# Kernel tuning notes

Measured on AMD Instinct MI355X. Metric: run time of the kernel, lower is better.

The kernel has to match this reference:

```python
import jax, jax.numpy as jnp
import numpy as np

CONF_THRES = 0.1
IOU_THRES = 0.6
MAX_DET = 300
MAX_WH = 4096.0  # class offset for non-agnostic NMS
NEG_SLOPE = 0.01  # nn.LeakyReLU default


def xywh2xyxy(p):
    xy, wh = p[..., :2], p[..., 2:4]
    return jnp.concatenate([xy - wh / 2, xy + wh / 2], axis=-1)


def pairwise_iou(a, b):
    area_a = (a[:, 2] - a[:, 0]) * (a[:, 3] - a[:, 1])
    area_b = (b[:, 2] - b[:, 0]) * (b[:, 3] - b[:, 1])
    lt = jnp.maximum(a[:, None, :2], b[None, :, :2])
    rb = jnp.minimum(a[:, None, 2:], b[None, :, 2:])
    wh = jnp.clip(rb - lt, 0.0)
    inter = wh[..., 0] * wh[..., 1]
    return inter / (area_a[:, None] + area_b[None, :] - inter + 1e-7)


def nms_single(pred):  # pred: [N, 5+nc]
    boxes = xywh2xyxy(pred[:, :4])
    scores = pred[:, 5:] * pred[:, 4:5]  # obj * cls
    conf = jnp.max(scores, axis=1)
    cls = jnp.argmax(scores, axis=1)
    conf = jnp.where(conf > CONF_THRES, conf, 0.0)
    topv, topi = jax.lax.top_k(conf, MAX_DET)
    b = boxes[topi]                      # [K,4]
    c = cls[topi]
    valid = topv > CONF_THRES
    bo = b + (c.astype(b.dtype) * MAX_WH)[:, None]  # class-offset boxes
    iou = pairwise_iou(bo, bo)           # [K,K]
    idx = jnp.arange(MAX_DET)
    def body(i, keep):
        sup = keep[i] & (iou[i] > IOU_THRES) & (idx > i)
        return keep & ~sup
    keep = jax.lax.fori_loop(0, MAX_DET, body, valid)
    return b, keep


def bilinear_sample(feat, y, x):  # feat [C,H,W], y/x [K,P] -> [C,K,P]
    C, H, W = feat.shape
    y = jnp.clip(y, 0.0, H - 1.0)
    x = jnp.clip(x, 0.0, W - 1.0)
    y0 = jnp.floor(y).astype(jnp.int32)
    x0 = jnp.floor(x).astype(jnp.int32)
    y1 = jnp.minimum(y0 + 1, H - 1)
    x1 = jnp.minimum(x0 + 1, W - 1)
    ly = y - y0
    lx = x - x0
    return (feat[:, y0, x0] * ((1 - ly) * (1 - lx))
            + feat[:, y0, x1] * ((1 - ly) * lx)
            + feat[:, y1, x0] * (ly * (1 - lx))
            + feat[:, y1, x1] * (ly * lx))


def roi_align_1x1(feat, boxes, scale):  # feat [C,H,W], boxes [K,4] xyxy (input-px)
    b = boxes * scale
    w = jnp.maximum(b[:, 2] - b[:, 0], 1.0)
    h = jnp.maximum(b[:, 3] - b[:, 1], 1.0)
    off = jnp.array([0.5, 1.5], dtype=boxes.dtype)
    xs = b[:, 0:1] + off[None, :] * (w[:, None] / 2.0)  # [K,2]
    ys = b[:, 1:2] + off[None, :] * (h[:, None] / 2.0)
    yy = ys[:, jnp.array([0, 0, 1, 1])]  # [K,4] 2x2 grid
    xx = xs[:, jnp.array([0, 1, 0, 1])]
    v = bilinear_sample(feat, yy, xx)    # [C,K,4]
    return jnp.mean(v, axis=2).T         # [K,C]


def rescale_boxes(bbox, hw, hw0):  # scale_coords + normalize by orig shape
    gain = jnp.minimum(hw[0] / hw0[0], hw[1] / hw0[1])
    pad_x = (hw[1] - hw0[1] * gain) / 2.0
    pad_y = (hw[0] - hw0[0] * gain) / 2.0
    x1 = jnp.clip((bbox[:, 0] - pad_x) / gain, 0.0, hw0[1])
    y1 = jnp.clip((bbox[:, 1] - pad_y) / gain, 0.0, hw0[0])
    x2 = jnp.clip((bbox[:, 2] - pad_x) / gain, 0.0, hw0[1])
    y2 = jnp.clip((bbox[:, 3] - pad_y) / gain, 0.0, hw0[0])
    # divide by shapes[i][0] indexed [w,h,w,h]
    return jnp.stack([x1 / hw0[1], y1 / hw0[0], x2 / hw0[1], y2 / hw0[0]], axis=1)


def setup_inputs() -> dict:
    key = jax.random.key(0)
    ks = jax.random.split(key, 10)
    B, N, NC = 8, 25500, 80
    xy = jax.random.uniform(ks[0], (B, N, 2), minval=0.0, maxval=640.0)
    wh = jax.random.uniform(ks[1], (B, N, 2), minval=8.0, maxval=160.0)
    obj = jax.random.uniform(ks[2], (B, N, 1))
    cls = jax.random.uniform(ks[3], (B, N, NC))
    preds = jnp.concatenate([xy, wh, obj, cls], axis=-1)
    feat1 = jax.random.normal(ks[4], (B, 128, 80, 80), dtype=jnp.float32)
    feat2 = jax.random.normal(ks[5], (B, 256, 40, 40), dtype=jnp.float32)
    feat3 = jax.random.normal(ks[6], (B, 512, 20, 20), dtype=jnp.float32)
    feat4 = jax.random.normal(ks[7], (B, 1024, 10, 10), dtype=jnp.float32)
    orig_hw = jnp.tile(jnp.array([[720.0, 1280.0]], dtype=jnp.float32), (B, 1))
    W1 = jax.random.normal(ks[8], (1920, 256), dtype=jnp.float32) * 0.02
    b1 = jnp.zeros((256,), dtype=jnp.float32)
    W2 = jax.random.normal(ks[9], (256, 256), dtype=jnp.float32) * 0.02
    b2 = jnp.zeros((256,), dtype=jnp.float32)
    return {"preds": preds, "feat1": feat1, "feat2": feat2, "feat3": feat3,
            "feat4": feat4, "orig_hw": orig_hw, "W1": W1, "b1": b1,
            "W2": W2, "b2": b2}


def reference(preds, feat1, feat2, feat3, feat4, orig_hw, W1, b1, W2, b2):
    preds = jax.lax.stop_gradient(preds)  # out.detach() in the original
    hw = jnp.array(feat1.shape[-2:], dtype=preds.dtype) * 8.0  # network input h,w
    boxes, keep = jax.vmap(nms_single)(preds)  # [B,K,4], [B,K]
    f1 = jax.vmap(lambda f, b: roi_align_1x1(f, b, 1.0 / 8))(feat1, boxes)
    f2 = jax.vmap(lambda f, b: roi_align_1x1(f, b, 1.0 / 16))(feat2, boxes)
    f3 = jax.vmap(lambda f, b: roi_align_1x1(f, b, 1.0 / 32))(feat3, boxes)
    f4 = jax.vmap(lambda f, b: roi_align_1x1(f, b, 1.0 / 64))(feat4, boxes)
    f = jnp.concatenate([f1, f2, f3, f4], axis=-1)  # [B,K,1920]
    h = jax.nn.leaky_relu(f @ W1 + b1, NEG_SLOPE)
    h = jax.nn.leaky_relu(h @ W2 + b2, NEG_SLOPE)   # [B,K,256]
    bb = jax.vmap(lambda b, s: rescale_boxes(b, hw, s))(boxes, orig_hw)
    out = jnp.concatenate([bb, h], axis=-1)  # [B,K,260]
    return out * keep[..., None].astype(out.dtype)
```

## Files before the change

### kernel.cpp

```cpp
#include <hip/hip_runtime.h>
#include <hip/hip_bf16.h>
#include <cstdint>
#include <cstddef>

#define NBATCH 8
#define NANCH 25500
#define MAXDET 300
#define NBINS 2048
#define SCAT_BLKS 64

typedef __bf16 bf16x8 __attribute__((ext_vector_type(8)));
typedef float floatx4 __attribute__((ext_vector_type(4)));
typedef unsigned long long ull;

__device__ __forceinline__ int conf_bin(float v) {
  unsigned bits = __float_as_uint(v);
  int bin = (int)((bits - 0x3D800000u) >> 14);
  return bin > (NBINS - 1) ? (NBINS - 1) : bin;
}

#define CONF_TILE 64
__global__ __launch_bounds__(256) void conf_kernel(const float* __restrict__ preds,
                                                   float* __restrict__ conf,
                                                   int* __restrict__ cls,
                                                   int* __restrict__ zmem, int zints,
                                                   int total) {
  if (blockIdx.x < 33) {
    int base = blockIdx.x * 1024;
    #pragma unroll
    for (int k = 0; k < 4; ++k) {
      int i = base + k * 256 + threadIdx.x;
      if (i < zints) zmem[i] = 0;
    }
  }
  __shared__ float s[CONF_TILE * 85];
  int base = blockIdx.x * CONF_TILE;
  int nA = total - base; if (nA > CONF_TILE) nA = CONF_TILE;
  int n4 = (nA * 85) >> 2;
  const float4* g4 = (const float4*)(preds + (size_t)base * 85);
  float4* s4 = (float4*)s;
  for (int i = threadIdx.x; i < n4; i += 256) s4[i] = g4[i];
  __syncthreads();
  int lane16 = threadIdx.x & 15;
  int sub = threadIdx.x >> 4;
  #pragma unroll
  for (int r = 0; r < 4; ++r) {
    int a = r * 16 + sub;
    if (a < nA) {
      const float* row = s + a * 85;
      float obj = row[4];
      float best = -1.0f; int bc = 0;
      #pragma unroll
      for (int j = 0; j < 5; ++j) {
        int c = lane16 * 5 + j;
        float v = row[5 + c] * obj;
        if (v > best) { best = v; bc = c; }
      }
      #pragma unroll
      for (int m = 1; m < 16; m <<= 1) {
        float ov = __shfl_xor(best, m, 64);
        int   oc = __shfl_xor(bc,   m, 64);
        if (ov > best || (ov == best && oc < bc)) { best = ov; bc = oc; }
      }
      if (lane16 == 0) {
        int idx = base + a;
        conf[idx] = (best > 0.1f) ? best : 0.0f;
        cls[idx] = bc;
      }
    }
  }
}

struct TransArgs {
  const float* src[6];
  __hip_bfloat16* dst[6];
  int C[6], HW[6], tx[6], tpb[6], start[6];
};

__global__ __launch_bounds__(256) void trans_scatter_kernel(TransArgs a,
                                                            const float* __restrict__ conf,
                                                            const float* __restrict__ preds,
                                                            const int* __restrict__ clsg,
                                                            int* __restrict__ ghist,
                                                            int* __restrict__ gcnt,
                                                            int* __restrict__ ctr1,
                                                            float* __restrict__ gV,
                                                            int* __restrict__ gI,
                                                            float4* __restrict__ gBox) {
  #pragma clang fp contract(off)
  __shared__ __align__(16) char smem[8448];
  int bid = blockIdx.x;
  int t = threadIdx.y * 32 + threadIdx.x;

  if (bid < SCAT_BLKS) {
    int b = bid >> 3, seg = bid & 7;
    int* s_h = (int*)smem;
    int* shv = (int*)(smem + 8192);
    #pragma unroll
    for (int k = 0; k < 8; ++k) s_h[t + k * 256] = 0;
    if (t == 0) shv[0] = NBINS;
    __syncthreads();
    const int N4 = NANCH >> 2;
    int i0 = (N4 * seg) >> 3, i1 = (N4 * (seg + 1)) >> 3;
    const float4* cf4 = (const float4*)(conf + (size_t)b * NANCH);
    for (int i = i0 + t; i < i1; i += 256) {
      float4 v = cf4[i];
      if (v.x > 0.1f) atomicAdd(&s_h[conf_bin(v.x)], 1);
      if (v.y > 0.1f) atomicAdd(&s_h[conf_bin(v.y)], 1);
      if (v.z > 0.1f) atomicAdd(&s_h[conf_bin(v.z)], 1);
      if (v.w > 0.1f) atomicAdd(&s_h[conf_bin(v.w)], 1);
    }
    __syncthreads();
    #pragma unroll
    for (int k = 0; k < 8; ++k) {
      int bin = t + k * 256;
      int c = s_h[bin];
      if (c) atomicAdd(&ghist[b * NBINS + bin], c);
    }
    __syncthreads();
    if (t == 0) {
      __threadfence();
      atomicAdd(&ctr1[b], 1);
      while (atomicAdd(&ctr1[b], 0) < 8) __builtin_amdgcn_s_sleep(2);
      __threadfence();
    }
    __syncthreads();
    int r[8], suf[8], rs[8];
    int w = t >> 6, lane = t & 63;
    {
      #pragma unroll
      for (int k = 0; k < 8; ++k)
        r[k] = atomicAdd(&ghist[b * NBINS + (w * 8 + k) * 64 + lane], 0);
      int bsum = 0;
      #pragma unroll
      for (int k = 0; k < 8; ++k) {
        int s = r[k];
        #pragma unroll
        for (int d = 1; d < 64; d <<= 1) {
          int o = __shfl_down(s, d, 64);
          if (lane + d < 64) s += o;
        }
        suf[k] = s - r[k];
        rs[k] = __shfl(s, 0, 64);
        bsum += rs[k];
      }
      if (lane == 0) shv[4 + w] = bsum;
    }
    __syncthreads();
    {
      int p1 = shv[5], p2 = shv[6], p3 = shv[7];
      int total = shv[4] + p1 + p2 + p3;
      int target = total < 300 ? total : 300;
      int RS = (w == 0) ? (p1 + p2 + p3) : (w == 1) ? (p2 + p3) : (w == 2) ? p3 : 0;
      int run = RS;
      #pragma unroll
      for (int k = 7; k >= 0; --k) {
        int Sx = run + suf[k] + r[k];
        int Sx1 = Sx - r[k];
        int bin = (w * 8 + k) * 64 + lane;
        s_h[bin] = Sx1;
        if (total > 0 && Sx >= target && Sx1 < target) shv[0] = bin;
        run += rs[k];
      }
    }
    __syncthreads();
    int T = shv[0];
    for (int i = i0 + t; i < i1; i += 256) {
      float4 v4 = cf4[i];
      int ib = i * 4;
      float vv[4] = {v4.x, v4.y, v4.z, v4.w};
      #pragma unroll
      for (int q = 0; q < 4; ++q) {
        float v = vv[q];
        if (v > 0.1f) {
          int bin = conf_bin(v);
          if (bin >= T) {
            int slot = s_h[bin] + atomicAdd(&gcnt[b * NBINS + bin], 1);
            int idx = ib + q;
            const float* p = preds + ((size_t)b * NANCH + idx) * 85;
            float cx = p[0], cy = p[1], wq = p[2], hq = p[3];
            float hw2 = wq * 0.5f, hh2 = hq * 0.5f;
            float x1 = cx - hw2, y1 = cy - hh2, x2 = cx + hw2, y2 = cy + hh2;
            int c = clsg[(size_t)b * NANCH + idx];
            size_t g = (size_t)b * NANCH + slot;
            gV[g] = v;
            gI[g] = idx | (c << 20);
            gBox[g] = make_float4(x1, y1, x2, y2);
          }
        }
      }
    }
    return;
  }

  {
    float (*tile)[33] = (float(*)[33])smem;
    int bid2 = bid - SCAT_BLKS;
    int s = 0;
    #pragma unroll
    for (int i = 1; i < 6; ++i) if (bid2 >= a.start[i]) s = i;
    int local = bid2 - a.start[s];
    int C = a.C[s], HW = a.HW[s], tx0 = a.tx[s], tpb = a.tpb[s];
    int b = local / tpb;
    int rem = local - b * tpb;
    int p0 = (rem % tx0) * 32;
    int c0 = (rem / tx0) * 32;
    const float* inb = a.src[s] + (size_t)b * C * HW;
    __hip_bfloat16* outb = a.dst[s] + (size_t)b * C * HW;
    int tx = threadIdx.x, ty = threadIdx.y;
    #pragma unroll
    for (int k = 0; k < 32; k += 8) {
      int c = c0 + ty + k, p = p0 + tx;
      if (c < C && p < HW) tile[ty + k][tx] = inb[(size_t)c * HW + p];
    }
    __syncthreads();
    #pragma unroll
    for (int k = 0; k < 32; k += 8) {
      int p = p0 + ty + k, c = c0 + tx;
      if (p < HW && c < C) outb[(size_t)p * C + c] = __float2bfloat16(tile[tx][ty + k]);
    }
  }
}

__global__ __launch_bounds__(1024) void nms_kernel(const float* __restrict__ gV,
                                                   const int* __restrict__ gI,
                                                   const float4* __restrict__ gBox,
                                                   const int* __restrict__ ghist,
                                                   float* __restrict__ boxesWs, int* __restrict__ keepWs,
                                                   const float* __restrict__ orig_hw,
                                                   float* __restrict__ out) {
  #pragma clang fp contract(off)
  __shared__ __align__(16) char smem[30208];
  int*    s_h  = (int*)smem;
  float4* bo4  = (float4*)(smem + 8192);
  float (*bxx)[4] = (float(*)[4])(smem + 12992);
  ull   (*mask)[5] = (ull(*)[5])(smem + 17792);
  ull* keepw = (ull*)(smem + 29792);
  ull* nzrow = (ull*)(smem + 29832);
  int* shv   = (int*)(smem + 29872);
  int b = blockIdx.x;
  int t = threadIdx.x;

  if (t < 300) {
    bo4[t] = make_float4(0.0f, 0.0f, 0.0f, 0.0f);
    bxx[t][0] = 0.0f; bxx[t][1] = 0.0f; bxx[t][2] = 0.0f; bxx[t][3] = 0.0f;
  }
  if (t < 5) nzrow[t] = 0ULL;
  if (t == 0) { shv[0] = NBINS; shv[2] = 0; }
  {
    int r[8], suf[8], rs[8];
    int w = t >> 6, lane = t & 63;
    if (t < 256) {
      #pragma unroll
      for (int k = 0; k < 8; ++k)
        r[k] = ghist[b * NBINS + (w * 8 + k) * 64 + lane];
      int bsum = 0;
      #pragma unroll
      for (int k = 0; k < 8; ++k) {
        int s = r[k];
        #pragma unroll
        for (int d = 1; d < 64; d <<= 1) {
          int o = __shfl_down(s, d, 64);
          if (lane + d < 64) s += o;
        }
        suf[k] = s - r[k];
        rs[k] = __shfl(s, 0, 64);
        bsum += rs[k];
      }
      if (lane == 0) shv[4 + w] = bsum;
    }
    __syncthreads();
    if (t < 256) {
      int p1 = shv[5], p2 = shv[6], p3 = shv[7];
      int total = shv[4] + p1 + p2 + p3;
      int target = total < 300 ? total : 300;
      int RS = (w == 0) ? (p1 + p2 + p3) : (w == 1) ? (p2 + p3) : (w == 2) ? p3 : 0;
      int run = RS;
      #pragma unroll
      for (int k = 7; k >= 0; --k) {
        int Sx = run + suf[k] + r[k];
        int Sx1 = Sx - r[k];
        int bin = (w * 8 + k) * 64 + lane;
        s_h[bin] = Sx;
        if (total > 0 && Sx >= target && Sx1 < target) { shv[0] = bin; shv[2] = Sx; }
        run += rs[k];
      }
      if (t == 0) shv[1] = total;
    }
  }
  __syncthreads();
  int total = shv[1];
  int Kslots = shv[2];
  int nvalid = total < 300 ? total : 300;

  if (t >= nvalid && t < 300) {
    size_t bi = ((size_t)(b * 300 + t)) * 4;
    boxesWs[bi + 0] = 0.0f; boxesWs[bi + 1] = 0.0f;
    boxesWs[bi + 2] = 0.0f; boxesWs[bi + 3] = 0.0f;
  }
  if (t < 5) {
    int n = nvalid - t * 64;
    keepw[t] = (n <= 0) ? 0ULL : (n >= 64 ? ~0ULL : ((1ULL << n) - 1ULL));
  }

  {
    const float* vb = gV + (size_t)b * NANCH;
    const int*   ib2 = gI + (size_t)b * NANCH;
    for (int sIdx = t; sIdx < Kslots; sIdx += 1024) {
      float v = vb[sIdx];
      unsigned code = (unsigned)ib2[sIdx];
      int id = (int)(code & 0xFFFFFu);
      int bin = conf_bin(v);
      int lo = (bin + 1 < NBINS) ? s_h[bin + 1] : 0;
      int hi = s_h[bin];
      int rank = lo;
      for (int j = lo; j < hi; ++j) {
        float vj = vb[j];
        int ij = ib2[j] & 0xFFFFF;
        int gt = vj > v;
        int eq = (vj == v) & (ij < id);
        rank += gt | eq;
      }
      if (rank < 300) {
        float4 bx = gBox[(size_t)b * NANCH + sIdx];
        bxx[rank][0] = bx.x; bxx[rank][1] = bx.y; bxx[rank][2] = bx.z; bxx[rank][3] = bx.w;
        size_t bi = ((size_t)(b * 300 + rank)) * 4;
        boxesWs[bi + 0] = bx.x; boxesWs[bi + 1] = bx.y;
        boxesWs[bi + 2] = bx.z; boxesWs[bi + 3] = bx.w;
        int c = (int)(code >> 20);
        float off = (float)c * 4096.0f;
        float4 ob; ob.x = bx.x + off; ob.y = bx.y + off; ob.z = bx.z + off; ob.w = bx.w + off;
        bo4[rank] = ob;
      }
    }
  }
  __syncthreads();

  {
    int wv2 = t >> 6, ln = t & 63;
    if (wv2 < 10) {
      int w2 = wv2 >> 1, half = wv2 & 1;
      int j = w2 * 64 + ln;
      int jc = j < 300 ? j : 0;
      float4 jb = bo4[jc];
      float ja = (jb.z - jb.x) * (jb.w - jb.y);
      bool jv = j < 300;
      int iend = w2 * 64 + 64; if (iend > 300) iend = 300;
      int i0 = half * 150, i1 = i0 + 150; if (i1 > iend) i1 = iend;
      #pragma unroll 4
      for (int i = i0; i < i1; ++i) {
        float4 ib = bo4[i];
        float ai = (ib.z - ib.x) * (ib.w - ib.y);
        float ltx = fmaxf(ib.x, jb.x);
        float lty = fmaxf(ib.y, jb.y);
        float rbx = fminf(ib.z, jb.z);
        float rby = fminf(ib.w, jb.w);
        float wx = fmaxf(rbx - ltx, 0.0f);
        float wy = fmaxf(rby - lty, 0.0f);
        float inter = wx * wy;
        float iou = inter / (ai + ja - inter + 1e-7f);
        ull bal = __ballot(jv && (j > i) && (iou > 0.6f));
        if (ln == 0) {
          mask[i][w2] = bal;
          if (bal) atomicOr(&nzrow[i >> 6], 1ULL << (i & 63));
        }
      }
    }
  }
  __syncthreads();
  if (t == 0) {
    ull kw[5], nz[5];
    #pragma unroll
    for (int w2 = 0; w2 < 5; ++w2) { kw[w2] = keepw[w2]; nz[w2] = nzrow[w2]; }
    #pragma unroll
    for (int w2 = 0; w2 < 5; ++w2) {
      ull p = kw[w2] & nz[w2];
      while (p) {
        int l2 = __builtin_ctzll(p);
        p &= p - 1;
        int i = w2 * 64 + l2;
        for (int w3 = w2; w3 < 5; ++w3) {
          ull m = mask[i][w3];
          kw[w3] &= ~m;
          if (w3 == w2) p &= ~m;
        }
      }
    }
    #pragma unroll
    for (int w2 = 0; w2 < 5; ++w2) keepw[w2] = kw[w2];
  }
  __syncthreads();
  if (t < 300) {
    int kp = (int)((keepw[t >> 6] >> (t & 63)) & 1ULL);
    keepWs[b * 300 + t] = kp;
    float oh = orig_hw[b * 2 + 0], ow = orig_hw[b * 2 + 1];
    float gain = fminf(640.0f / oh, 640.0f / ow);
    float padx = (640.0f - ow * gain) * 0.5f;
    float pady = (640.0f - oh * gain) * 0.5f;
    float x1 = fminf(fmaxf((bxx[t][0] - padx) / gain, 0.0f), ow) / ow;
    float y1 = fminf(fmaxf((bxx[t][1] - pady) / gain, 0.0f), oh) / oh;
    float x2 = fminf(fmaxf((bxx[t][2] - padx) / gain, 0.0f), ow) / ow;
    float y2 = fminf(fmaxf((bxx[t][3] - pady) / gain, 0.0f), oh) / oh;
    size_t o = ((size_t)(b * 300 + t)) * 260;
    out[o + 0] = kp ? x1 : 0.0f;
    out[o + 1] = kp ? y1 : 0.0f;
    out[o + 2] = kp ? x2 : 0.0f;
    out[o + 3] = kp ? y2 : 0.0f;
  }
}

__global__ __launch_bounds__(256) void roi_kernel(const float* __restrict__ boxes,
                                                  const __hip_bfloat16* __restrict__ fT1, const __hip_bfloat16* __restrict__ fT2,
                                                  const __hip_bfloat16* __restrict__ fT3, const __hip_bfloat16* __restrict__ fT4,
                                                  __hip_bfloat16* __restrict__ f) {
  int b = blockIdx.x & 7;
  int r = blockIdx.x >> 3;
  __shared__ int t_off[4][16];
  __shared__ float t_w[4][16];
  int t = threadIdx.x;
  const int Hs[4] = {80, 40, 20, 10};
  const int Cs[4] = {128, 256, 512, 1024};
  const float ss[4] = {0.125f, 0.0625f, 0.03125f, 0.015625f};
  size_t bbase = ((size_t)(b * 300 + r)) * 4;
  float bx0 = boxes[bbase + 0];
  float by0 = boxes[bbase + 1];
  float bx1 = boxes[bbase + 2];
  float by1 = boxes[bbase + 3];
  if (t < 64) {
    int lv = t >> 4, k = t & 15, pp = k >> 2, nb = k & 3;
    float s = ss[lv];
    int H = Hs[lv], W = Hs[lv], C = Cs[lv];
    float b0 = bx0 * s, b1 = by0 * s, b2 = bx1 * s, b3 = by1 * s;
    float w = fmaxf(b2 - b0, 1.0f), h = fmaxf(b3 - b1, 1.0f);
    const float offv[2] = {0.5f, 1.5f};
    float px = b0 + offv[pp & 1] * (w * 0.5f);
    float py = b1 + offv[pp >> 1] * (h * 0.5f);
    float y = fminf(fmaxf(py, 0.0f), (float)(H - 1));
    float x = fminf(fmaxf(px, 0.0f), (float)(W - 1));
    int y0 = (int)floorf(y), x0 = (int)floorf(x);
    int y1 = min(y0 + 1, H - 1), x1 = min(x0 + 1, W - 1);
    float ly = y - (float)y0, lx = x - (float)x0;
    int yy = (nb & 2) ? y1 : y0;
    int xx = (nb & 1) ? x1 : x0;
    float wy = (nb & 2) ? ly : (1.0f - ly);
    float wx = (nb & 1) ? lx : (1.0f - lx);
    t_off[lv][k] = (yy * W + xx) * C;
    t_w[lv][k] = wy * wx;
  }
  __syncthreads();
  const __hip_bfloat16* bases[4] = {
    fT1 + (size_t)b * 6400 * 128,
    fT2 + (size_t)b * 1600 * 256,
    fT3 + (size_t)b * 400 * 512,
    fT4 + (size_t)b * 100 * 1024
  };
  __hip_bfloat16* frow = f + (size_t)(b * 300 + r) * 1920;
  int cbase = 0;
  #pragma unroll
  for (int lv = 0; lv < 4; ++lv) {
    int C = Cs[lv];
    const __hip_bfloat16* base = bases[lv];
    for (int c = t; c < C; c += 256) {
      float acc = 0.0f;
      #pragma unroll
      for (int k = 0; k < 16; ++k)
        acc += t_w[lv][k] * __bfloat162float(base[t_off[lv][k] + c]);
      frow[cbase + c] = __float2bfloat16(acc * 0.25f);
    }
    cbase += C;
  }
}

#define GLDS16(gp, lp) __builtin_amdgcn_global_load_lds( \
    (const __attribute__((address_space(1))) unsigned int*)(gp), \
    (__attribute__((address_space(3))) unsigned int*)(lp), 16, 0, 0)

__global__ __launch_bounds__(256) void gemm_tile_kernel(const __hip_bfloat16* __restrict__ A,
                                                        const __hip_bfloat16* __restrict__ BT,
                                                        const float* __restrict__ bias,
                                                        __hip_bfloat16* __restrict__ Cb,
                                                        float* __restrict__ Cf,
                                                        const int* __restrict__ keep,
                                                        int M, int N, int K, int ldc, int coff) {
  __shared__ __hip_bfloat16 sA[2][64 * 64];
  __shared__ __hip_bfloat16 sB[2][64 * 64];
  int tid = threadIdx.x;
  int bm = blockIdx.x * 64, bn = blockIdx.y * 64;
  int wave = tid >> 6, lane = tid & 63;
  int wr = wave >> 1, wc = wave & 1;
  int idx16 = lane & 15, kb = lane >> 4;
  floatx4 acc[2][2] = {};
  int nt = K >> 6;

  auto stage = [&](int buf, int t) {
    int k0 = t << 6;
    #pragma unroll
    for (int i = 0; i < 2; ++i) {
      int c = tid + i * 256;
      int row = c >> 3, cc = c & 7;
      int scc = cc ^ (row & 7);
      GLDS16(A + (size_t)(bm + row) * K + k0 + scc * 8,
             (char*)&sA[buf][0] + c * 16);
    }
    #pragma unroll
    for (int i = 0; i < 2; ++i) {
      int c = tid + i * 256;
      int row = c >> 3, cc = c & 7;
      int scc = cc ^ (row & 7);
      GLDS16(BT + (size_t)(bn + row) * K + k0 + scc * 8,
             (char*)&sB[buf][0] + c * 16);
    }
  };

  stage(0, 0);
  asm volatile("s_waitcnt vmcnt(0)" ::: "memory");
  __syncthreads();
  int cur = 0;
  for (int t = 0; t < nt; ++t) {
    if (t + 1 < nt) stage(cur ^ 1, t + 1);
    const char* Ab = (const char*)&sA[cur][0];
    const char* Bb = (const char*)&sB[cur][0];
    #pragma unroll
    for (int s = 0; s < 2; ++s) {
      bf16x8 af[2], bg[2];
      #pragma unroll
      for (int m = 0; m < 2; ++m) {
        int row = wr * 32 + m * 16 + idx16;
        int chunk = s * 4 + kb;
        af[m] = *(const bf16x8*)(Ab + row * 128 + ((chunk ^ (row & 7)) * 16));
      }
      #pragma unroll
      for (int n = 0; n < 2; ++n) {
        int row = wc * 32 + n * 16 + idx16;
        int chunk = s * 4 + kb;
        bg[n] = *(const bf16x8*)(Bb + row * 128 + ((chunk ^ (row & 7)) * 16));
      }
      #pragma unroll
      for (int m = 0; m < 2; ++m)
        #pragma unroll
        for (int n = 0; n < 2; ++n)
          acc[m][n] = __builtin_amdgcn_mfma_f32_16x16x32_bf16(af[m], bg[n], acc[m][n], 0, 0, 0);
    }
    asm volatile("s_waitcnt vmcnt(0)" ::: "memory");
    __syncthreads();
    cur ^= 1;
  }
  int col = lane & 15, rb4 = (lane >> 4) * 4;
  #pragma unroll
  for (int m = 0; m < 2; ++m) {
    #pragma unroll
    for (int n = 0; n < 2; ++n) {
      #pragma unroll
      for (int r = 0; r < 4; ++r) {
        int orow = bm + wr * 32 + m * 16 + rb4 + r;
        int ocol = bn + wc * 32 + n * 16 + col;
        if (orow >= M) continue;
        float v = acc[m][n][r] + bias[ocol];
        v = (v >= 0.0f) ? v : 0.01f * v;
        if (Cb) Cb[(size_t)orow * N + ocol] = __float2bfloat16(v);
        if (Cf) {
          float km = keep ? (keep[orow] ? 1.0f : 0.0f) : 1.0f;
          Cf[(size_t)orow * ldc + coff + ocol] = v * km;
        }
      }
    }
  }
}

extern "C" void kernel_launch(void* const* d_in, const int* in_sizes, int n_in,
                              void* d_out, int out_size, void* d_ws, size_t ws_size,
                              hipStream_t stream) {
  (void)in_sizes; (void)n_in; (void)out_size; (void)ws_size;
  const float* preds  = (const float*)d_in[0];
  const float* feat1  = (const float*)d_in[1];
  const float* feat2  = (const float*)d_in[2];
  const float* feat3  = (const float*)d_in[3];
  const float* feat4  = (const float*)d_in[4];
  const float* orighw = (const float*)d_in[5];
  const float* W1     = (const float*)d_in[6];
  const float* b1     = (const float*)d_in[7];
  const float* W2     = (const float*)d_in[8];
  const float* b2     = (const float*)d_in[9];
  float* out = (float*)d_out;

  char* ws = (char*)d_ws;
  size_t off = 0;
  auto alloc = [&](size_t bytes) -> void* {
    void* p = ws + off;
    off = (off + bytes + 255) & ~(size_t)255;
    return p;
  };
  const int BN = NBATCH * NANCH;
  float*  conf   = (float*)alloc((size_t)BN * 4);
  int*    cls    = (int*)  alloc((size_t)BN * 4);
  float*  gV     = (float*)alloc((size_t)BN * 4);
  int*    gI     = (int*)  alloc((size_t)BN * 4);
  float4* gBox   = (float4*)alloc((size_t)BN * 16);
  int*    ghist  = (int*)  alloc((size_t)NBATCH * NBINS * 4);
  int*    gcnt   = (int*)  alloc((size_t)NBATCH * NBINS * 4);
  int*    ctr1   = (int*)  alloc(256);
  const int zints = NBATCH * NBINS * 2 + 64;
  float*  boxes  = (float*)alloc((size_t)NBATCH * 300 * 4 * 4);
  int*    keep   = (int*)  alloc((size_t)NBATCH * 300 * 4);
  __hip_bfloat16* fT1  = (__hip_bfloat16*)alloc((size_t)NBATCH * 6400 * 128 * 2);
  __hip_bfloat16* fT2  = (__hip_bfloat16*)alloc((size_t)NBATCH * 1600 * 256 * 2);
  __hip_bfloat16* fT3  = (__hip_bfloat16*)alloc((size_t)NBATCH * 400 * 512 * 2);
  __hip_bfloat16* fT4  = (__hip_bfloat16*)alloc((size_t)NBATCH * 100 * 1024 * 2);
  __hip_bfloat16* fmat = (__hip_bfloat16*)alloc((size_t)2400 * 1920 * 2);
  __hip_bfloat16* h1b  = (__hip_bfloat16*)alloc((size_t)2400 * 256 * 2);
  __hip_bfloat16* W1T  = (__hip_bfloat16*)alloc((size_t)256 * 1920 * 2);
  __hip_bfloat16* W2T  = (__hip_bfloat16*)alloc((size_t)256 * 256 * 2);

  conf_kernel<<<(BN + CONF_TILE - 1) / CONF_TILE, 256, 0, stream>>>(preds, conf, cls,
                                                                    ghist, zints, BN);

  TransArgs ta;
  ta.src[0] = feat1; ta.dst[0] = fT1; ta.C[0] = 128;  ta.HW[0] = 6400; ta.tx[0] = 200;
  ta.src[1] = feat2; ta.dst[1] = fT2; ta.C[1] = 256;  ta.HW[1] = 1600; ta.tx[1] = 50;
  ta.src[2] = feat3; ta.dst[2] = fT3; ta.C[2] = 512;  ta.HW[2] = 400;  ta.tx[2] = 13;
  ta.src[3] = feat4; ta.dst[3] = fT4; ta.C[3] = 1024; ta.HW[3] = 100;  ta.tx[3] = 4;
  ta.src[4] = W1;    ta.dst[4] = W1T; ta.C[4] = 1920; ta.HW[4] = 256;  ta.tx[4] = 8;
  ta.src[5] = W2;    ta.dst[5] = W2T; ta.C[5] = 256;  ta.HW[5] = 256;  ta.tx[5] = 8;
  int n_tiles = 0;
  for (int s = 0; s < 6; ++s) {
    int ty = (ta.C[s] + 31) / 32;
    int nbatch = (s < 4) ? NBATCH : 1;
    ta.tpb[s] = ta.tx[s] * ty;
    ta.start[s] = n_tiles;
    n_tiles += ta.tpb[s] * nbatch;
  }
  trans_scatter_kernel<<<SCAT_BLKS + n_tiles, dim3(32, 8), 0, stream>>>(ta, conf, preds, cls,
                                                                        ghist, gcnt, ctr1,
                                                                        gV, gI, gBox);

  nms_kernel<<<NBATCH, 1024, 0, stream>>>(gV, gI, gBox, ghist, boxes, keep, orighw, out);

  roi_kernel<<<2400, 256, 0, stream>>>(boxes, fT1, fT2, fT3, fT4, fmat);
  gemm_tile_kernel<<<dim3(38, 4), 256, 0, stream>>>(fmat, W1T, b1, h1b, nullptr, nullptr,
                                                    2400, 256, 1920, 0, 0);
  gemm_tile_kernel<<<dim3(38, 4), 256, 0, stream>>>(h1b, W2T, b2, nullptr, out, keep,
                                                    2400, 256, 256, 260, 4);
}
```

Baseline: 133.3 us.

## Split scatter into its own kernel and fuse NMS with the feature transposes

The scatter work moves out of the transpose kernel into a standalone 64-block kernel. The per-batch NMS now runs in 256-thread blocks that share a launch with the feature and weight transposes, so NMS overlaps the transpose traffic instead of sitting as a separate serial launch. The transpose uses 64x64 tiles with float4 loads and 16-byte bf16 stores. The serial single-thread suppression sweep is replaced by a wave-level loop that finds the lowest pending index with a shuffle min-reduction. The risk is that NMS in 256-thread blocks does more work per thread, and the larger shared-memory footprint may reduce occupancy for the transpose blocks.

```diff
diff --git a/kernel.cpp b/kernel.cpp
--- a/kernel.cpp
+++ b/kernel.cpp
@@ -12,6 +12,8 @@
 typedef __bf16 bf16x8 __attribute__((ext_vector_type(8)));
 typedef float floatx4 __attribute__((ext_vector_type(4)));
 typedef unsigned long long ull;
+
+struct __align__(16) bfvec8 { __hip_bfloat16 h[8]; };
 
 __device__ __forceinline__ int conf_bin(float v) {
   unsigned bits = __float_as_uint(v);
@@ -71,66 +73,214 @@
   }
 }
 
+__global__ __launch_bounds__(256) void scatter_kernel(const float* __restrict__ conf,
+                                                      const float* __restrict__ preds,
+                                                      const int* __restrict__ clsg,
+                                                      int* __restrict__ ghist,
+                                                      int* __restrict__ gcnt,
+                                                      int* __restrict__ ctr1,
+                                                      float* __restrict__ gV,
+                                                      int* __restrict__ gI,
+                                                      float4* __restrict__ gBox) {
+  #pragma clang fp contract(off)
+  __shared__ __align__(16) char smem[8448];
+  int bid = blockIdx.x;
+  int t = threadIdx.x;
+  int b = bid >> 3, seg = bid & 7;
+  int* s_h = (int*)smem;
+  int* shv = (int*)(smem + 8192);
+  #pragma unroll
+  for (int k = 0; k < 8; ++k) s_h[t + k * 256] = 0;
+  if (t == 0) shv[0] = NBINS;
+  __syncthreads();
+  const int N4 = NANCH >> 2;
+  int i0 = (N4 * seg) >> 3, i1 = (N4 * (seg + 1)) >> 3;
+  const float4* cf4 = (const float4*)(conf + (size_t)b * NANCH);
+  for (int i = i0 + t; i < i1; i += 256) {
+    float4 v = cf4[i];
+    if (v.x > 0.1f) atomicAdd(&s_h[conf_bin(v.x)], 1);
+    if (v.y > 0.1f) atomicAdd(&s_h[conf_bin(v.y)], 1);
+    if (v.z > 0.1f) atomicAdd(&s_h[conf_bin(v.z)], 1);
+    if (v.w > 0.1f) atomicAdd(&s_h[conf_bin(v.w)], 1);
+  }
+  __syncthreads();
+  #pragma unroll
+  for (int k = 0; k < 8; ++k) {
+    int bin = t + k * 256;
+    int c = s_h[bin];
+    if (c) atomicAdd(&ghist[b * NBINS + bin], c);
+  }
+  __syncthreads();
+  if (t == 0) {
+    __threadfence();
+    atomicAdd(&ctr1[b], 1);
+    while (atomicAdd(&ctr1[b], 0) < 8) __builtin_amdgcn_s_sleep(2);
+    __threadfence();
+  }
+  __syncthreads();
+  int r[8], suf[8], rs[8];
+  int w = t >> 6, lane = t & 63;
+  {
+    #pragma unroll
+    for (int k = 0; k < 8; ++k)
+      r[k] = atomicAdd(&ghist[b * NBINS + (w * 8 + k) * 64 + lane], 0);
+    int bsum = 0;
+    #pragma unroll
+    for (int k = 0; k < 8; ++k) {
+      int s = r[k];
+      #pragma unroll
+      for (int d = 1; d < 64; d <<= 1) {
+        int o = __shfl_down(s, d, 64);
+        if (lane + d < 64) s += o;
+      }
+      suf[k] = s - r[k];
+      rs[k] = __shfl(s, 0, 64);
+      bsum += rs[k];
+    }
+    if (lane == 0) shv[4 + w] = bsum;
+  }
+  __syncthreads();
+  {
+    int p1 = shv[5], p2 = shv[6], p3 = shv[7];
+    int total = shv[4] + p1 + p2 + p3;
+    int target = total < 300 ? total : 300;
+    int RS = (w == 0) ? (p1 + p2 + p3) : (w == 1) ? (p2 + p3) : (w == 2) ? p3 : 0;
+    int run = RS;
+    #pragma unroll
+    for (int k = 7; k >= 0; --k) {
+      int Sx = run + suf[k] + r[k];
+      int Sx1 = Sx - r[k];
+      int bin = (w * 8 + k) * 64 + lane;
+      s_h[bin] = Sx1;
+      if (total > 0 && Sx >= target && Sx1 < target) shv[0] = bin;
+      run += rs[k];
+    }
+  }
+  __syncthreads();
+  int T = shv[0];
+  for (int i = i0 + t; i < i1; i += 256) {
+    float4 v4 = cf4[i];
+    int ib = i * 4;
+    float vv[4] = {v4.x, v4.y, v4.z, v4.w};
+    #pragma unroll
+    for (int q = 0; q < 4; ++q) {
+      float v = vv[q];
+      if (v > 0.1f) {
+        int bin = conf_bin(v);
+        if (bin >= T) {
+          int slot = s_h[bin] + atomicAdd(&gcnt[b * NBINS + bin], 1);
+          int idx = ib + q;
+          const float* p = preds + ((size_t)b * NANCH + idx) * 85;
+          float cx = p[0], cy = p[1], wq = p[2], hq = p[3];
+          float hw2 = wq * 0.5f, hh2 = hq * 0.5f;
+          float x1 = cx - hw2, y1 = cy - hh2, x2 = cx + hw2, y2 = cy + hh2;
+          int c = clsg[(size_t)b * NANCH + idx];
+          size_t g = (size_t)b * NANCH + slot;
+          gV[g] = v;
+          gI[g] = idx | (c << 20);
+          gBox[g] = make_float4(x1, y1, x2, y2);
+        }
+      }
+    }
+  }
+}
+
 struct TransArgs {
   const float* src[6];
   __hip_bfloat16* dst[6];
   int C[6], HW[6], tx[6], tpb[6], start[6];
 };
 
-__global__ __launch_bounds__(256) void trans_scatter_kernel(TransArgs a,
-                                                            const float* __restrict__ conf,
-                                                            const float* __restrict__ preds,
-                                                            const int* __restrict__ clsg,
-                                                            int* __restrict__ ghist,
-                                                            int* __restrict__ gcnt,
-                                                            int* __restrict__ ctr1,
-                                                            float* __restrict__ gV,
-                                                            int* __restrict__ gI,
-                                                            float4* __restrict__ gBox) {
+__global__ __launch_bounds__(256) void nms_trans_kernel(TransArgs a,
+                                                        const float* __restrict__ gV,
+                                                        const int* __restrict__ gI,
+                                                        const float4* __restrict__ gBox,
+                                                        const int* __restrict__ ghist,
+                                                        float* __restrict__ boxesWs, int* __restrict__ keepWs,
+                                                        const float* __restrict__ orig_hw,
+                                                        float* __restrict__ out) {
   #pragma clang fp contract(off)
-  __shared__ __align__(16) char smem[8448];
+  __shared__ __align__(16) char smem[30208];
   int bid = blockIdx.x;
-  int t = threadIdx.y * 32 + threadIdx.x;
-
-  if (bid < SCAT_BLKS) {
-    int b = bid >> 3, seg = bid & 7;
-    int* s_h = (int*)smem;
-    int* shv = (int*)(smem + 8192);
-    #pragma unroll
-    for (int k = 0; k < 8; ++k) s_h[t + k * 256] = 0;
-    if (t == 0) shv[0] = NBINS;
+  int t = threadIdx.x;
+
+  if (bid >= 8) {
+    float (*tile)[65] = (float(*)[65])smem;
+    int bid2 = bid - 8;
+    int s = 0;
+    #pragma unroll
+    for (int i = 1; i < 6; ++i) if (bid2 >= a.start[i]) s = i;
+    int local = bid2 - a.start[s];
+    int C = a.C[s], HW = a.HW[s], txp = a.tx[s], tpb = a.tpb[s];
+    int b = local / tpb;
+    int rem = local - b * tpb;
+    int p0 = (rem % txp) * 64;
+    int c0 = (rem / txp) * 64;
+    const float* inb = a.src[s] + (size_t)b * C * HW;
+    __hip_bfloat16* outb = a.dst[s] + (size_t)b * C * HW;
+    int rgrp = t >> 4, cg = t & 15;
+    if (p0 + 64 <= HW) {
+      #pragma unroll
+      for (int k = 0; k < 4; ++k) {
+        int r = k * 16 + rgrp;
+        float4 v = *(const float4*)(inb + (size_t)(c0 + r) * HW + p0 + cg * 4);
+        tile[r][cg * 4 + 0] = v.x; tile[r][cg * 4 + 1] = v.y;
+        tile[r][cg * 4 + 2] = v.z; tile[r][cg * 4 + 3] = v.w;
+      }
+    } else {
+      int nvp = HW - p0;
+      #pragma unroll
+      for (int k = 0; k < 4; ++k) {
+        int r = k * 16 + rgrp;
+        const float* src = inb + (size_t)(c0 + r) * HW + p0;
+        #pragma unroll
+        for (int j = 0; j < 4; ++j) {
+          int pp = cg * 4 + j;
+          tile[r][pp] = (pp < nvp) ? src[pp] : 0.0f;
+        }
+      }
+    }
     __syncthreads();
-    const int N4 = NANCH >> 2;
-    int i0 = (N4 * seg) >> 3, i1 = (N4 * (seg + 1)) >> 3;
-    const float4* cf4 = (const float4*)(conf + (size_t)b * NANCH);
-    for (int i = i0 + t; i < i1; i += 256) {
-      float4 v = cf4[i];
-      if (v.x > 0.1f) atomicAdd(&s_h[conf_bin(v.x)], 1);
-      if (v.y > 0.1f) atomicAdd(&s_h[conf_bin(v.y)], 1);
-      if (v.z > 0.1f) atomicAdd(&s_h[conf_bin(v.z)], 1);
-      if (v.w > 0.1f) atomicAdd(&s_h[conf_bin(v.w)], 1);
-    }
-    __syncthreads();
-    #pragma unroll
-    for (int k = 0; k < 8; ++k) {
-      int bin = t + k * 256;
-      int c = s_h[bin];
-      if (c) atomicAdd(&ghist[b * NBINS + bin], c);
-    }
-    __syncthreads();
-    if (t == 0) {
-      __threadfence();
-      atomicAdd(&ctr1[b], 1);
-      while (atomicAdd(&ctr1[b], 0) < 8) __builtin_amdgcn_s_sleep(2);
-      __threadfence();
-    }
-    __syncthreads();
+    int cb = (t & 7) * 8;
+    #pragma unroll
+    for (int pass = 0; pass < 2; ++pass) {
+      int p = pass * 32 + (t >> 3);
+      if (p0 + p < HW) {
+        bfvec8 o;
+        #pragma unroll
+        for (int j = 0; j < 8; ++j) o.h[j] = __float2bfloat16(tile[cb + j][p]);
+        *(bfvec8*)(outb + (size_t)(p0 + p) * C + c0 + cb) = o;
+      }
+    }
+    return;
+  }
+
+  int*    s_h  = (int*)smem;
+  float4* bo4  = (float4*)(smem + 8192);
+  float (*bxx)[4] = (float(*)[4])(smem + 12992);
+  ull   (*mask)[5] = (ull(*)[5])(smem + 17792);
+  ull* keepw = (ull*)(smem + 29792);
+  ull* nzrow = (ull*)(smem + 29832);
+  int* shv   = (int*)(smem + 29872);
+  int b = bid;
+
+  for (int i = t; i < 300; i += 256) {
+    bo4[i] = make_float4(0.0f, 0.0f, 0.0f, 0.0f);
+    bxx[i][0] = 0.0f; bxx[i][1] = 0.0f; bxx[i][2] = 0.0f; bxx[i][3] = 0.0f;
+  }
+  {
+    ull* mflat = (ull*)(smem + 17792);
+    for (int i = t; i < 1500; i += 256) mflat[i] = 0ULL;
+  }
+  if (t < 5) nzrow[t] = 0ULL;
+  if (t == 0) { shv[0] = NBINS; shv[2] = 0; }
+  {
     int r[8], suf[8], rs[8];
     int w = t >> 6, lane = t & 63;
     {
       #pragma unroll
       for (int k = 0; k < 8; ++k)
-        r[k] = atomicAdd(&ghist[b * NBINS + (w * 8 + k) * 64 + lane], 0);
+        r[k] = ghist[b * NBINS + (w * 8 + k) * 64 + lane];
       int bsum = 0;
       #pragma unroll
       for (int k = 0; k < 8; ++k) {
@@ -158,129 +308,6 @@
         int Sx = run + suf[k] + r[k];
         int Sx1 = Sx - r[k];
         int bin = (w * 8 + k) * 64 + lane;
-        s_h[bin] = Sx1;
-        if (total > 0 && Sx >= target && Sx1 < target) shv[0] = bin;
-        run += rs[k];
-      }
-    }
-    __syncthreads();
-    int T = shv[0];
-    for (int i = i0 + t; i < i1; i += 256) {
-      float4 v4 = cf4[i];
-      int ib = i * 4;
-      float vv[4] = {v4.x, v4.y, v4.z, v4.w};
-      #pragma unroll
-      for (int q = 0; q < 4; ++q) {
-        float v = vv[q];
-        if (v > 0.1f) {
-          int bin = conf_bin(v);
-          if (bin >= T) {
-            int slot = s_h[bin] + atomicAdd(&gcnt[b * NBINS + bin], 1);
-            int idx = ib + q;
-            const float* p = preds + ((size_t)b * NANCH + idx) * 85;
-            float cx = p[0], cy = p[1], wq = p[2], hq = p[3];
-            float hw2 = wq * 0.5f, hh2 = hq * 0.5f;
-            float x1 = cx - hw2, y1 = cy - hh2, x2 = cx + hw2, y2 = cy + hh2;
-            int c = clsg[(size_t)b * NANCH + idx];
-            size_t g = (size_t)b * NANCH + slot;
-            gV[g] = v;
-            gI[g] = idx | (c << 20);
-            gBox[g] = make_float4(x1, y1, x2, y2);
-          }
-        }
-      }
-    }
-    return;
-  }
-
-  {
-    float (*tile)[33] = (float(*)[33])smem;
-    int bid2 = bid - SCAT_BLKS;
-    int s = 0;
-    #pragma unroll
-    for (int i = 1; i < 6; ++i) if (bid2 >= a.start[i]) s = i;
-    int local = bid2 - a.start[s];
-    int C = a.C[s], HW = a.HW[s], tx0 = a.tx[s], tpb = a.tpb[s];
-    int b = local / tpb;
-    int rem = local - b * tpb;
-    int p0 = (rem % tx0) * 32;
-    int c0 = (rem / tx0) * 32;
-    const float* inb = a.src[s] + (size_t)b * C * HW;
-    __hip_bfloat16* outb = a.dst[s] + (size_t)b * C * HW;
-    int tx = threadIdx.x, ty = threadIdx.y;
-    #pragma unroll
-    for (int k = 0; k < 32; k += 8) {
-      int c = c0 + ty + k, p = p0 + tx;
-      if (c < C && p < HW) tile[ty + k][tx] = inb[(size_t)c * HW + p];
-    }
-    __syncthreads();
-    #pragma unroll
-    for (int k = 0; k < 32; k += 8) {
-      int p = p0 + ty + k, c = c0 + tx;
-      if (p < HW && c < C) outb[(size_t)p * C + c] = __float2bfloat16(tile[tx][ty + k]);
-    }
-  }
-}
-
-__global__ __launch_bounds__(1024) void nms_kernel(const float* __restrict__ gV,
-                                                   const int* __restrict__ gI,
-                                                   const float4* __restrict__ gBox,
-                                                   const int* __restrict__ ghist,
-                                                   float* __restrict__ boxesWs, int* __restrict__ keepWs,
-                                                   const float* __restrict__ orig_hw,
-                                                   float* __restrict__ out) {
-  #pragma clang fp contract(off)
-  __shared__ __align__(16) char smem[30208];
-  int*    s_h  = (int*)smem;
-  float4* bo4  = (float4*)(smem + 8192);
-  float (*bxx)[4] = (float(*)[4])(smem + 12992);
-  ull   (*mask)[5] = (ull(*)[5])(smem + 17792);
-  ull* keepw = (ull*)(smem + 29792);
-  ull* nzrow = (ull*)(smem + 29832);
-  int* shv   = (int*)(smem + 29872);
-  int b = blockIdx.x;
-  int t = threadIdx.x;
-
-  if (t < 300) {
-    bo4[t] = make_float4(0.0f, 0.0f, 0.0f, 0.0f);
-    bxx[t][0] = 0.0f; bxx[t][1] = 0.0f; bxx[t][2] = 0.0f; bxx[t][3] = 0.0f;
-  }
-  if (t < 5) nzrow[t] = 0ULL;
-  if (t == 0) { shv[0] = NBINS; shv[2] = 0; }
-  {
-    int r[8], suf[8], rs[8];
-    int w = t >> 6, lane = t & 63;
-    if (t < 256) {
-      #pragma unroll
-      for (int k = 0; k < 8; ++k)
-        r[k] = ghist[b * NBINS + (w * 8 + k) * 64 + lane];
-      int bsum = 0;
-      #pragma unroll
-      for (int k = 0; k < 8; ++k) {
-        int s = r[k];
-        #pragma unroll
-        for (int d = 1; d < 64; d <<= 1) {
-          int o = __shfl_down(s, d, 64);
-          if (lane + d < 64) s += o;
-        }
-        suf[k] = s - r[k];
-        rs[k] = __shfl(s, 0, 64);
-        bsum += rs[k];
-      }
-      if (lane == 0) shv[4 + w] = bsum;
-    }
-    __syncthreads();
-    if (t < 256) {
-      int p1 = shv[5], p2 = shv[6], p3 = shv[7];
-      int total = shv[4] + p1 + p2 + p3;
-      int target = total < 300 ? total : 300;
-      int RS = (w == 0) ? (p1 + p2 + p3) : (w == 1) ? (p2 + p3) : (w == 2) ? p3 : 0;
-      int run = RS;
-      #pragma unroll
-      for (int k = 7; k >= 0; --k) {
-        int Sx = run + suf[k] + r[k];
-        int Sx1 = Sx - r[k];
-        int bin = (w * 8 + k) * 64 + lane;
         s_h[bin] = Sx;
         if (total > 0 && Sx >= target && Sx1 < target) { shv[0] = bin; shv[2] = Sx; }
         run += rs[k];
@@ -293,10 +320,12 @@
   int Kslots = shv[2];
   int nvalid = total < 300 ? total : 300;
 
-  if (t >= nvalid && t < 300) {
-    size_t bi = ((size_t)(b * 300 + t)) * 4;
-    boxesWs[bi + 0] = 0.0f; boxesWs[bi + 1] = 0.0f;
-    boxesWs[bi + 2] = 0.0f; boxesWs[bi + 3] = 0.0f;
+  for (int i = t; i < 300; i += 256) {
+    if (i >= nvalid) {
+      size_t bi = ((size_t)(b * 300 + i)) * 4;
+      boxesWs[bi + 0] = 0.0f; boxesWs[bi + 1] = 0.0f;
+      boxesWs[bi + 2] = 0.0f; boxesWs[bi + 3] = 0.0f;
+    }
   }
   if (t < 5) {
     int n = nvalid - t * 64;
@@ -306,7 +335,7 @@
   {
     const float* vb = gV + (size_t)b * NANCH;
     const int*   ib2 = gI + (size_t)b * NANCH;
-    for (int sIdx = t; sIdx < Kslots; sIdx += 1024) {
+    for (int sIdx = t; sIdx < Kslots; sIdx += 256) {
       float v = vb[sIdx];
       unsigned code = (unsigned)ib2[sIdx];
       int id = (int)(code & 0xFFFFFu);
@@ -338,8 +367,8 @@
 
   {
     int wv2 = t >> 6, ln = t & 63;
-    if (wv2 < 10) {
-      int w2 = wv2 >> 1, half = wv2 & 1;
+    for (int task = wv2; task < 10; task += 4) {
+      int w2 = task >> 1, half = task & 1;
       int j = w2 * 64 + ln;
       int jc = j < 300 ? j : 0;
       float4 jb = bo4[jc];
@@ -368,40 +397,42 @@
     }
   }
   __syncthreads();
-  if (t == 0) {
-    ull kw[5], nz[5];
-    #pragma unroll
-    for (int w2 = 0; w2 < 5; ++w2) { kw[w2] = keepw[w2]; nz[w2] = nzrow[w2]; }
-    #pragma unroll
-    for (int w2 = 0; w2 < 5; ++w2) {
-      ull p = kw[w2] & nz[w2];
-      while (p) {
-        int l2 = __builtin_ctzll(p);
-        p &= p - 1;
-        int i = w2 * 64 + l2;
-        for (int w3 = w2; w3 < 5; ++w3) {
-          ull m = mask[i][w3];
-          kw[w3] &= ~m;
-          if (w3 == w2) p &= ~m;
-        }
-      }
-    }
-    #pragma unroll
-    for (int w2 = 0; w2 < 5; ++w2) keepw[w2] = kw[w2];
-  }
-  __syncthreads();
-  if (t < 300) {
-    int kp = (int)((keepw[t >> 6] >> (t & 63)) & 1ULL);
-    keepWs[b * 300 + t] = kp;
+
+  if (t < 64) {
+    int l = t;
+    ull kw_l = (l < 5) ? keepw[l] : 0ULL;
+    ull nz_l = (l < 5) ? nzrow[l] : 0ULL;
+    ull pend = kw_l & nz_l;
+    for (;;) {
+      int cand = pend ? (l * 64 + (int)__builtin_ctzll(pend)) : 0x7FFFFFFF;
+      int m = cand;
+      #pragma unroll
+      for (int d = 1; d < 64; d <<= 1) {
+        int o = __shfl_xor(m, d, 64);
+        m = o < m ? o : m;
+      }
+      if (m == 0x7FFFFFFF) break;
+      ull msk = (l < 5 && l >= (m >> 6)) ? mask[m][l] : 0ULL;
+      kw_l &= ~msk;
+      if (l == (m >> 6)) pend &= ~(1ULL << (m & 63));
+      pend &= ~msk;
+      pend &= kw_l;
+    }
+    if (l < 5) keepw[l] = kw_l;
+  }
+  __syncthreads();
+  for (int i = t; i < 300; i += 256) {
+    int kp = (int)((keepw[i >> 6] >> (i & 63)) & 1ULL);
+    keepWs[b * 300 + i] = kp;
     float oh = orig_hw[b * 2 + 0], ow = orig_hw[b * 2 + 1];
     float gain = fminf(640.0f / oh, 640.0f / ow);
     float padx = (640.0f - ow * gain) * 0.5f;
     float pady = (640.0f - oh * gain) * 0.5f;
-    float x1 = fminf(fmaxf((bxx[t][0] - padx) / gain, 0.0f), ow) / ow;
-    float y1 = fminf(fmaxf((bxx[t][1] - pady) / gain, 0.0f), oh) / oh;
-    float x2 = fminf(fmaxf((bxx[t][2] - padx) / gain, 0.0f), ow) / ow;
-    float y2 = fminf(fmaxf((bxx[t][3] - pady) / gain, 0.0f), oh) / oh;
-    size_t o = ((size_t)(b * 300 + t)) * 260;
+    float x1 = fminf(fmaxf((bxx[i][0] - padx) / gain, 0.0f), ow) / ow;
+    float y1 = fminf(fmaxf((bxx[i][1] - pady) / gain, 0.0f), oh) / oh;
+    float x2 = fminf(fmaxf((bxx[i][2] - padx) / gain, 0.0f), ow) / ow;
+    float y2 = fminf(fmaxf((bxx[i][3] - pady) / gain, 0.0f), oh) / oh;
+    size_t o = ((size_t)(b * 300 + i)) * 260;
     out[o + 0] = kp ? x1 : 0.0f;
     out[o + 1] = kp ? y1 : 0.0f;
     out[o + 2] = kp ? x2 : 0.0f;
@@ -614,26 +645,28 @@
   conf_kernel<<<(BN + CONF_TILE - 1) / CONF_TILE, 256, 0, stream>>>(preds, conf, cls,
                                                                     ghist, zints, BN);
 
+  scatter_kernel<<<SCAT_BLKS, 256, 0, stream>>>(conf, preds, cls, ghist, gcnt, ctr1,
+                                                gV, gI, gBox);
+
   TransArgs ta;
-  ta.src[0] = feat1; ta.dst[0] = fT1; ta.C[0] = 128;  ta.HW[0] = 6400; ta.tx[0] = 200;
-  ta.src[1] = feat2; ta.dst[1] = fT2; ta.C[1] = 256;  ta.HW[1] = 1600; ta.tx[1] = 50;
-  ta.src[2] = feat3; ta.dst[2] = fT3; ta.C[2] = 512;  ta.HW[2] = 400;  ta.tx[2] = 13;
-  ta.src[3] = feat4; ta.dst[3] = fT4; ta.C[3] = 1024; ta.HW[3] = 100;  ta.tx[3] = 4;
-  ta.src[4] = W1;    ta.dst[4] = W1T; ta.C[4] = 1920; ta.HW[4] = 256;  ta.tx[4] = 8;
-  ta.src[5] = W2;    ta.dst[5] = W2T; ta.C[5] = 256;  ta.HW[5] = 256;  ta.tx[5] = 8;
+  ta.src[0] = feat1; ta.dst[0] = fT1; ta.C[0] = 128;  ta.HW[0] = 6400;
+  ta.src[1] = feat2; ta.dst[1] = fT2; ta.C[1] = 256;  ta.HW[1] = 1600;
+  ta.src[2] = feat3; ta.dst[2] = fT3; ta.C[2] = 512;  ta.HW[2] = 400;
+  ta.src[3] = feat4; ta.dst[3] = fT4; ta.C[3] = 1024; ta.HW[3] = 100;
+  ta.src[4] = W1;    ta.dst[4] = W1T; ta.C[4] = 1920; ta.HW[4] = 256;
+  ta.src[5] = W2;    ta.dst[5] = W2T; ta.C[5] = 256;  ta.HW[5] = 256;
   int n_tiles = 0;
   for (int s = 0; s < 6; ++s) {
-    int ty = (ta.C[s] + 31) / 32;
+    int txp = (ta.HW[s] + 63) / 64;
+    int tyc = ta.C[s] / 64;
     int nbatch = (s < 4) ? NBATCH : 1;
-    ta.tpb[s] = ta.tx[s] * ty;
+    ta.tx[s] = txp;
+    ta.tpb[s] = txp * tyc;
     ta.start[s] = n_tiles;
     n_tiles += ta.tpb[s] * nbatch;
   }
-  trans_scatter_kernel<<<SCAT_BLKS + n_tiles, dim3(32, 8), 0, stream>>>(ta, conf, preds, cls,
-                                                                        ghist, gcnt, ctr1,
-                                                                        gV, gI, gBox);
-
-  nms_kernel<<<NBATCH, 1024, 0, stream>>>(gV, gI, gBox, ghist, boxes, keep, orighw, out);
+  nms_trans_kernel<<<8 + n_tiles, 256, 0, stream>>>(ta, gV, gI, gBox, ghist,
+                                                    boxes, keep, orighw, out);
 
   roi_kernel<<<2400, 256, 0, stream>>>(boxes, fT1, fT2, fT3, fT4, fmat);
   gemm_tile_kernel<<<dim3(38, 4), 256, 0, stream>>>(fmat, W1T, b1, h1b, nullptr, nullptr,
```

New measurement: 162.5 us. 21.9% more time.
